# Kernel optimization log

Measured on AMD Instinct MI355X. Metric: run time of the kernel, lower is better.

The kernel has to match this reference:

```python
import jax, jax.numpy as jnp
import numpy as np

DIM = 1024


def setup_inputs() -> dict:
    key = jax.random.key(0)
    ks = jax.random.split(key, 9)
    s = 1.0 / np.sqrt(DIM)
    x = jax.random.normal(ks[0], (4, 4096, DIM), dtype=jnp.float32)
    Wq = jax.random.uniform(ks[1], (DIM, DIM), jnp.float32, -s, s)
    bq = jax.random.uniform(ks[2], (DIM,), jnp.float32, -s, s)
    Wk = jax.random.uniform(ks[3], (DIM, DIM), jnp.float32, -s, s)
    bk = jax.random.uniform(ks[4], (DIM,), jnp.float32, -s, s)
    Wv = jax.random.uniform(ks[5], (DIM, DIM), jnp.float32, -s, s)
    bv = jax.random.uniform(ks[6], (DIM,), jnp.float32, -s, s)
    Wo = jax.random.uniform(ks[7], (DIM, DIM), jnp.float32, -s, s)
    bo = jax.random.uniform(ks[8], (DIM,), jnp.float32, -s, s)
    return {"x": x, "Wq": Wq, "bq": bq, "Wk": Wk, "bk": bk,
            "Wv": Wv, "bv": bv, "Wo": Wo, "bo": bo}


def reference(x, Wq, bq, Wk, bk, Wv, bv, Wo, bo):
    # x: [B, N, C]; weights stored as [C, C] (torch Linear applies x @ W.T,
    # here we store W already transposed so x @ W matches).
    scale = x.shape[-1] ** (-0.5)
    q = x @ Wq + bq                                  # [B, N, C]
    k = x @ Wk + bk
    v = x @ Wv + bv
    scores = jnp.einsum('bnc,bmc->bnm', q, k) * scale  # [B, N, N]
    attn = jax.nn.softmax(scores, axis=-1)
    out = jnp.einsum('bnm,bmc->bnc', attn, v)          # [B, N, C]
    return out @ Wo + bo
```

## Files before the change

### kernel.cpp

```cpp
#include <hip/hip_runtime.h>
#include <hip/hip_bf16.h>
#include <stdint.h>

typedef __bf16 bf16_8 __attribute__((ext_vector_type(8)));
typedef float  f32x4  __attribute__((ext_vector_type(4)));

#define GLL(g, l) __builtin_amdgcn_global_load_lds(                         \
    (__attribute__((address_space(1))) void*)(g),                           \
    (__attribute__((address_space(3))) void*)(l), 16, 0, 0)

__global__ void sniff_dtype(const uint32_t* __restrict__ x, uint32_t* __restrict__ flag)
{
    uint32_t w = x[threadIdx.x];
    uint32_t e = (w >> 23) & 0xFF;
    int isf32 = (e >= 100 && e <= 145) ? 1 : 0;
    unsigned long long m = __ballot(isf32);
    if (threadIdx.x == 0) *flag = (__popcll(m) >= 48) ? 1u : 0u;
}

__global__ __launch_bounds__(256)
void convert_to_bf16(const void* __restrict__ in, long elemOff,
                     __bf16* __restrict__ out, long n, const uint32_t* __restrict__ flag)
{
    long i = ((long)blockIdx.x * 256 + threadIdx.x) * 8;
    if (i >= n) return;
    bf16_8 o;
    if (*flag) {
        const float* p = (const float*)in + elemOff + i;
        float4 a = *(const float4*)p;
        float4 b = *(const float4*)(p + 4);
        o[0]=(__bf16)a.x; o[1]=(__bf16)a.y; o[2]=(__bf16)a.z; o[3]=(__bf16)a.w;
        o[4]=(__bf16)b.x; o[5]=(__bf16)b.y; o[6]=(__bf16)b.z; o[7]=(__bf16)b.w;
    } else {
        o = *(const bf16_8*)((const __bf16*)in + elemOff + i);
    }
    *(bf16_8*)(out + i) = o;
}

__global__ __launch_bounds__(256)
void convert_bias4(const void* b0, const void* b1, const void* b2, const void* b3,
                   __bf16* o0, __bf16* o1, __bf16* o2, __bf16* o3,
                   const uint32_t* __restrict__ flag)
{
    const void* in = (blockIdx.x == 0) ? b0 : (blockIdx.x == 1) ? b1
                   : (blockIdx.x == 2) ? b2 : b3;
    __bf16* out = (blockIdx.x == 0) ? o0 : (blockIdx.x == 1) ? o1
                : (blockIdx.x == 2) ? o2 : o3;
    long i = (long)threadIdx.x * 8;
    if (i >= 1024) return;
    bf16_8 o;
    if (*flag) {
        const float* p = (const float*)in + i;
        float4 a = *(const float4*)p;
        float4 b = *(const float4*)(p + 4);
        o[0]=(__bf16)a.x; o[1]=(__bf16)a.y; o[2]=(__bf16)a.z; o[3]=(__bf16)a.w;
        o[4]=(__bf16)b.x; o[5]=(__bf16)b.y; o[6]=(__bf16)b.z; o[7]=(__bf16)b.w;
    } else {
        o = *(const bf16_8*)((const __bf16*)in + i);
    }
    *(bf16_8*)(out + i) = o;
}

__global__ __launch_bounds__(256)
void convT_w4(const void* W0, const void* W1, const void* W2, const void* W3,
              __bf16* T0, __bf16* T1, __bf16* T2, __bf16* T3,
              const uint32_t* __restrict__ flag)
{
    const void* W = (blockIdx.z == 0) ? W0 : (blockIdx.z == 1) ? W1
                  : (blockIdx.z == 2) ? W2 : W3;
    __bf16* WT    = (blockIdx.z == 0) ? T0 : (blockIdx.z == 1) ? T1
                  : (blockIdx.z == 2) ? T2 : T3;
    __shared__ __bf16 tile[64][72];
    const int bc = blockIdx.x * 64, br = blockIdx.y * 64;
    const int c = threadIdx.x & 63, r0 = threadIdx.x >> 6;
    const bool f32 = (*flag != 0);
#pragma unroll
    for (int i = 0; i < 16; i++) {
        int r = i * 4 + r0;
        long idx = (long)(br + r) * 1024 + bc + c;
        float v = f32 ? ((const float*)W)[idx] : (float)((const __bf16*)W)[idx];
        tile[r][c] = (__bf16)v;
    }
    __syncthreads();
#pragma unroll
    for (int i = 0; i < 16; i++) {
        int r = i * 4 + r0;
        WT[(long)(bc + r) * 1024 + br + c] = tile[c][r];
    }
}

template<int BN_T, int OUT_MODE, bool HAS_BIAS>
__global__ __launch_bounds__(256)
void gemm_bt(const __bf16* __restrict__ A, int lda,
             const __bf16* __restrict__ BT, int ldb,
             void* __restrict__ C, int ldc,
             const __bf16* __restrict__ bias,
             int M, int N, int kLen, long zCbytes, float scale,
             float* __restrict__ rowSums)
{
    constexpr int NT    = (BN_T == 128) ? 4 : 2;
    constexpr int BHALF = BN_T * 32;
    __shared__ __align__(16) __bf16 As[2 * 128 * 32];
    __shared__ __align__(16) __bf16 Bs[2 * BHALF];

    const int t    = threadIdx.x;
    const int wave = t >> 6;
    const int lane = t & 63;
    const int quad = lane >> 4;
    const int lrow = lane & 15;
    const int wm   = wave >> 1;
    const int wn   = wave & 1;
    const long m0  = (long)blockIdx.y * 128;
    const long n0  = (long)blockIdx.x * BN_T;

    A  += (long)blockIdx.z * kLen;
    BT += (long)blockIdx.z * kLen;
    C   = (void*)((char*)C + (long)blockIdx.z * zCbytes);

    const int sr = lane >> 2;
    const int sc = (lane & 3) ^ ((lane >> 3) & 3);

    const __bf16* aSrc = A + (m0 + wave * 32 + sr) * (long)lda + sc * 8;
    const __bf16* bSrc = (BN_T == 128)
        ? BT + (n0 + wave * 32 + sr) * (long)ldb + sc * 8
        : BT + (n0 + wave * 16 + sr) * (long)ldb + sc * 8;
    __bf16* aDst = As + wave * 1024;
    __bf16* bDst = Bs + wave * (BN_T == 128 ? 1024 : 512);
    const long a16 = 16L * lda, b16 = 16L * ldb;

    f32x4 zero4 = {0.f, 0.f, 0.f, 0.f};
    f32x4 acc[4][NT];
#pragma unroll
    for (int mt = 0; mt < 4; mt++)
#pragma unroll
        for (int nt = 0; nt < NT; nt++) acc[mt][nt] = zero4;

    const int sl = (lrow >> 1) & 3;

    for (int k0 = 0; k0 < kLen; k0 += 64) {
        GLL(aSrc, aDst);
        GLL(aSrc + a16, aDst + 512);
        GLL(bSrc, bDst);
        if (BN_T == 128) GLL(bSrc + b16, bDst + 512);
        GLL(aSrc + 32, aDst + 4096);
        GLL(aSrc + a16 + 32, aDst + 4096 + 512);
        GLL(bSrc + 32, bDst + BHALF);
        if (BN_T == 128) GLL(bSrc + b16 + 32, bDst + BHALF + 512);
        aSrc += 64; bSrc += 64;
        __syncthreads();

#pragma unroll
        for (int kk = 0; kk < 2; kk++) {
            bf16_8 af[4], bfr[NT];
#pragma unroll
            for (int mt = 0; mt < 4; mt++)
                af[mt] = *(const bf16_8*)(As + kk * 4096
                           + (wm * 64 + mt * 16 + lrow) * 32 + (quad ^ sl) * 8);
#pragma unroll
            for (int nt = 0; nt < NT; nt++)
                bfr[nt] = *(const bf16_8*)(Bs + kk * BHALF
                           + (wn * (BN_T / 2) + nt * 16 + lrow) * 32 + (quad ^ sl) * 8);

#pragma unroll
            for (int mt = 0; mt < 4; mt++)
#pragma unroll
                for (int nt = 0; nt < NT; nt++)
                    acc[mt][nt] = __builtin_amdgcn_mfma_f32_16x16x32_bf16(
                                      af[mt], bfr[nt], acc[mt][nt], 0, 0, 0);
        }
        __syncthreads();
    }

    if (OUT_MODE == 3) {
#pragma unroll
        for (int mt = 0; mt < 4; mt++) {
#pragma unroll
            for (int i = 0; i < 4; i++) {
                long row = m0 + wm * 64 + mt * 16 + quad * 4 + i;
                float rs = 0.f;
#pragma unroll
                for (int nt = 0; nt < NT; nt++) {
                    long col = n0 + wn * (BN_T / 2) + nt * 16 + lrow;
                    float e = exp2f(acc[mt][nt][i] * scale);
                    ((__bf16*)C)[row * (long)ldc + col] = (__bf16)e;
                    rs += e;
                }
                rs += __shfl_xor(rs, 1);
                rs += __shfl_xor(rs, 2);
                rs += __shfl_xor(rs, 4);
                rs += __shfl_xor(rs, 8);
                if (lrow == 0) atomicAdd(&rowSums[row], rs);
            }
        }
        return;
    }

#pragma unroll
    for (int mt = 0; mt < 4; mt++) {
#pragma unroll
        for (int nt = 0; nt < NT; nt++) {
#pragma unroll
            for (int i = 0; i < 4; i++) {
                long row = m0 + wm * 64 + mt * 16 + quad * 4 + i;
                long col = n0 + wn * (BN_T / 2) + nt * 16 + lrow;
                float v = acc[mt][nt][i] * scale;
                if (HAS_BIAS) v += (float)bias[col];
                if (OUT_MODE == 0)      ((__bf16*)C)[row * (long)ldc + col] = (__bf16)v;
                else if (OUT_MODE == 1) ((__bf16*)C)[col * (long)ldc + row] = (__bf16)v;
                else                    ((float* )C)[row * (long)ldc + col] = v;
            }
        }
    }
}

__global__ __launch_bounds__(256)
void softmax_f32_to_bf16(float* __restrict__ S)
{
    float* srow = S + (long)blockIdx.x * 4096;
    __bf16* prow = (__bf16*)srow;
    const int t  = threadIdx.x;
    const int wv = t >> 6, ln = t & 63;

    float4 vv[4];
    float m = -1e30f;
#pragma unroll
    for (int i = 0; i < 4; i++) {
        vv[i] = ((const float4*)srow)[t + i * 256];
        m = fmaxf(m, fmaxf(fmaxf(vv[i].x, vv[i].y), fmaxf(vv[i].z, vv[i].w)));
    }
#pragma unroll
    for (int o = 32; o; o >>= 1) m = fmaxf(m, __shfl_xor(m, o));
    __shared__ float redm[4];
    if (ln == 0) redm[wv] = m;
    __syncthreads();
    m = fmaxf(fmaxf(redm[0], redm[1]), fmaxf(redm[2], redm[3]));

    const float L2E = 1.4426950408889634f;
    float s = 0.f;
#pragma unroll
    for (int i = 0; i < 4; i++) {
        vv[i].x = exp2f((vv[i].x - m) * L2E);
        vv[i].y = exp2f((vv[i].y - m) * L2E);
        vv[i].z = exp2f((vv[i].z - m) * L2E);
        vv[i].w = exp2f((vv[i].w - m) * L2E);
        s += vv[i].x + vv[i].y + vv[i].z + vv[i].w;
    }
#pragma unroll
    for (int o = 32; o; o >>= 1) s += __shfl_xor(s, o);
    __shared__ float reds[4];
    if (ln == 0) reds[wv] = s;
    __syncthreads();
    s = reds[0] + reds[1] + reds[2] + reds[3];
    float inv = 1.f / s;

    __syncthreads();
#pragma unroll
    for (int i = 0; i < 4; i++) {
        long base = (long)(t + i * 256) * 4;
        prow[base + 0] = (__bf16)(vv[i].x * inv);
        prow[base + 1] = (__bf16)(vv[i].y * inv);
        prow[base + 2] = (__bf16)(vv[i].z * inv);
        prow[base + 3] = (__bf16)(vv[i].w * inv);
    }
}

__global__ __launch_bounds__(256)
void reduce2_to_bf16(const float* __restrict__ Sf, __bf16* __restrict__ ao)
{
    const long i = blockIdx.x;
    const float* p = Sf + 4096 * i + 2048;
    const int t = threadIdx.x;
    float4 a = ((const float4*)p)[t];
    float4 b = ((const float4*)(p + 1024))[t];
    __bf16* o = ao + i * 1024 + t * 4;
    o[0] = (__bf16)(a.x + b.x);
    o[1] = (__bf16)(a.y + b.y);
    o[2] = (__bf16)(a.z + b.z);
    o[3] = (__bf16)(a.w + b.w);
}

__global__ __launch_bounds__(256)
void reduce2_scaled(const float* __restrict__ part, const float* __restrict__ sums,
                    __bf16* __restrict__ ao)
{
    const long i = blockIdx.x;
    const float inv = 1.0f / sums[i];
    const float* p = part + i * 2048;
    const int t = threadIdx.x;
    float4 a = ((const float4*)p)[t];
    float4 b = ((const float4*)(p + 1024))[t];
    __bf16* o = ao + i * 1024 + t * 4;
    o[0] = (__bf16)((a.x + b.x) * inv);
    o[1] = (__bf16)((a.y + b.y) * inv);
    o[2] = (__bf16)((a.z + b.z) * inv);
    o[3] = (__bf16)((a.w + b.w) * inv);
}

__global__ void fill_const_f32(float* p, long n, float val)
{
    long i = (long)blockIdx.x * 256 + threadIdx.x;
    if (i < n) p[i] = val;
}

extern "C" void kernel_launch(void* const* d_in, const int* in_sizes, int n_in,
                              void* d_out, int out_size, void* d_ws, size_t ws_size,
                              hipStream_t stream)
{
    const void* x  = d_in[0];
    const void* Wq = d_in[1];
    const void* bq = d_in[2];
    const void* Wk = d_in[3];
    const void* bk = d_in[4];
    const void* Wv = d_in[5];
    const void* bv = d_in[6];
    const void* Wo = d_in[7];
    const void* bo = d_in[8];

    const int  Bb = 4, Nn = 4096, Cc = 1024;
    const long seqB = (long)Nn * Cc;
    const long allR = (long)Bb * Nn;

    auto pad = [](size_t b) { return (b + 255) & ~(size_t)255; };
    const size_t szW    = (size_t)Cc * Cc * 2;
    const size_t szBias = (size_t)Cc * 2;
    const size_t szSeq  = (size_t)seqB * 2;
    const size_t szAll  = (size_t)allR * Cc * 2;

    const size_t fixed = pad(256) + 4 * pad(szW) + 4 * pad(szBias) + pad(szAll);
    const size_t needB = fixed + 4 * pad(szSeq);
    const size_t needA = fixed + 4 * pad(szAll);

    dim3 blk(256);

    if (ws_size < needB) {
        float val = 3000.0f + (float)(ws_size >> 20);
        fill_const_f32<<<dim3((out_size + 255) / 256), blk, 0, stream>>>(
            (float*)d_out, out_size, val);
        return;
    }

    const bool batched = (ws_size >= needA);

    char* ws = (char*)d_ws;
    size_t off = 0;
    auto alloc = [&](size_t bytes) -> char* { char* p = ws + off; off += pad(bytes); return p; };

    uint32_t* flag = (uint32_t*)alloc(256);
    __bf16* WqT = (__bf16*)alloc(szW);
    __bf16* WkT = (__bf16*)alloc(szW);
    __bf16* WvT = (__bf16*)alloc(szW);
    __bf16* WoT = (__bf16*)alloc(szW);
    __bf16* bqc = (__bf16*)alloc(szBias);
    __bf16* bkc = (__bf16*)alloc(szBias);
    __bf16* bvc = (__bf16*)alloc(szBias);
    __bf16* boc = (__bf16*)alloc(szBias);
    __bf16* ao  = (__bf16*)alloc(szAll);
    const size_t tierSz = batched ? szAll : szSeq;
    __bf16* xc  = (__bf16*)alloc(tierSz);
    __bf16* q   = (__bf16*)alloc(tierSz);
    __bf16* k   = (__bf16*)alloc(tierSz);
    __bf16* vT  = (__bf16*)alloc(tierSz);

    sniff_dtype<<<dim3(1), dim3(64), 0, stream>>>((const uint32_t*)x, flag);
    convT_w4<<<dim3(16, 16, 4), blk, 0, stream>>>(Wq, Wk, Wv, Wo, WqT, WkT, WvT, WoT, flag);
    convert_bias4<<<dim3(4), blk, 0, stream>>>(bq, bk, bv, bo, bqc, bkc, bvc, boc, flag);

    const float scale    = 0.03125f;
    const float scaleL2E = 0.03125f * 1.4426950408889634f;

    if (batched) {
        convert_to_bf16<<<dim3(allR * Cc / 2048), blk, 0, stream>>>(x, 0, xc, allR * Cc, flag);
        dim3 gProj(Cc / 128, allR / 128);
        gemm_bt<128, 0, true><<<gProj, blk, 0, stream>>>(xc, Cc, WqT, Cc, q,  Cc,  bqc, (int)allR, Cc, Cc, 0, 1.f, nullptr);
        gemm_bt<128, 0, true><<<gProj, blk, 0, stream>>>(xc, Cc, WkT, Cc, k,  Cc,  bkc, (int)allR, Cc, Cc, 0, 1.f, nullptr);
        gemm_bt<128, 1, true><<<gProj, blk, 0, stream>>>(xc, Cc, WvT, Cc, vT, (int)allR, bvc, (int)allR, Cc, Cc, 0, 1.f, nullptr);

        float* sums4 = (float*)xc;
        fill_const_f32<<<dim3(64), blk, 0, stream>>>(sums4, 4L * Nn, 0.f);

        __bf16* P   = (__bf16*)d_out;
        float* part = (float*)((char*)d_out + (size_t)Nn * Nn * 2);

        for (int b = 0; b < Bb; b++) {
            const __bf16* qb  = q + (long)b * seqB;
            const __bf16* kb  = k + (long)b * seqB;
            const __bf16* vTb = vT + (long)b * Nn;
            float* sums = sums4 + (long)b * Nn;

            gemm_bt<128, 3, false><<<dim3(Nn / 128, Nn / 128), blk, 0, stream>>>(
                qb, Cc, kb, Cc, P, Nn, nullptr, Nn, Nn, Cc, 0, scaleL2E, sums);

            gemm_bt<128, 2, false><<<dim3(Cc / 128, Nn / 128, 2), blk, 0, stream>>>(
                P, Nn, vTb, (int)allR, part, 2048,
                nullptr, Nn, Cc, Nn / 2, 4096 , 1.f, nullptr);

            reduce2_scaled<<<dim3(Nn), blk, 0, stream>>>(
                part, sums, ao + (long)b * seqB);
        }
    } else {
        float* S = (float*)d_out;
        for (int b = 0; b < Bb; b++) {
            convert_to_bf16<<<dim3(seqB / 2048), blk, 0, stream>>>(x, b * seqB, xc, seqB, flag);
            dim3 gProj(Cc / 64, Nn / 128);
            gemm_bt<64, 0, true><<<gProj, blk, 0, stream>>>(xc, Cc, WqT, Cc, q,  Cc, bqc, Nn, Cc, Cc, 0, 1.f, nullptr);
            gemm_bt<64, 0, true><<<gProj, blk, 0, stream>>>(xc, Cc, WkT, Cc, k,  Cc, bkc, Nn, Cc, Cc, 0, 1.f, nullptr);
            gemm_bt<64, 1, true><<<gProj, blk, 0, stream>>>(xc, Cc, WvT, Cc, vT, Nn, bvc, Nn, Cc, Cc, 0, 1.f, nullptr);

            gemm_bt<128, 2, false><<<dim3(Nn / 128, Nn / 128), blk, 0, stream>>>(
                q, Cc, k, Cc, S, Nn, nullptr, Nn, Nn, Cc, 0, scale, nullptr);

            softmax_f32_to_bf16<<<dim3(Nn), blk, 0, stream>>>(S);

            gemm_bt<128, 2, false><<<dim3(Cc / 128, Nn / 128, 2), blk, 0, stream>>>(
                (const __bf16*)S, 2 * Nn, vT, Nn, (float*)S + 2048, Nn,
                nullptr, Nn, Cc, Nn / 2, 4096, 1.f, nullptr);

            reduce2_to_bf16<<<dim3(Nn), blk, 0, stream>>>(S, ao + (long)b * seqB);
        }
    }

    gemm_bt<128, 2, true><<<dim3(Cc / 128, (int)(allR / 128)), blk, 0, stream>>>(
        ao, Cc, WoT, Cc, (float*)d_out, Cc, boc, (int)allR, Cc, Cc, 0, 1.f, nullptr);
}
```

Baseline: 847.3 us.

## Double-buffer LDS tiles in bf16 GEMM to overlap global loads with MFMA

Adds a second LDS buffer for the A and B tiles so the direct global-to-LDS loads for the next K step are issued before the MFMA work on the current step. This removes one barrier per iteration and hides load latency behind compute. Wave priority is also raised around the MFMA section. In exchange LDS use per block doubles, which can lower occupancy, and completion of the prefetch relies on the barrier's implicit wait.

```diff
diff --git a/kernel.cpp b/kernel.cpp
--- a/kernel.cpp
+++ b/kernel.cpp
@@ -100,8 +100,8 @@
 {
     constexpr int NT    = (BN_T == 128) ? 4 : 2;
     constexpr int BHALF = BN_T * 32;
-    __shared__ __align__(16) __bf16 As[2 * 128 * 32];
-    __shared__ __align__(16) __bf16 Bs[2 * BHALF];
+    __shared__ __align__(16) __bf16 As[2][2 * 128 * 32];
+    __shared__ __align__(16) __bf16 Bs[2][2 * BHALF];
 
     const int t    = threadIdx.x;
     const int wave = t >> 6;
@@ -124,8 +124,6 @@
     const __bf16* bSrc = (BN_T == 128)
         ? BT + (n0 + wave * 32 + sr) * (long)ldb + sc * 8
         : BT + (n0 + wave * 16 + sr) * (long)ldb + sc * 8;
-    __bf16* aDst = As + wave * 1024;
-    __bf16* bDst = Bs + wave * (BN_T == 128 ? 1024 : 512);
     const long a16 = 16L * lda, b16 = 16L * ldb;
 
     f32x4 zero4 = {0.f, 0.f, 0.f, 0.f};
@@ -137,28 +135,30 @@
 
     const int sl = (lrow >> 1) & 3;
 
-    for (int k0 = 0; k0 < kLen; k0 += 64) {
-        GLL(aSrc, aDst);
-        GLL(aSrc + a16, aDst + 512);
-        GLL(bSrc, bDst);
-        if (BN_T == 128) GLL(bSrc + b16, bDst + 512);
-        GLL(aSrc + 32, aDst + 4096);
-        GLL(aSrc + a16 + 32, aDst + 4096 + 512);
-        GLL(bSrc + 32, bDst + BHALF);
-        if (BN_T == 128) GLL(bSrc + b16 + 32, bDst + BHALF + 512);
-        aSrc += 64; bSrc += 64;
-        __syncthreads();
-
+    auto STAGE = [&](int buf, const __bf16* aS, const __bf16* bS) {
+        __bf16* aD = &As[buf][0] + wave * 1024;
+        __bf16* bD = &Bs[buf][0] + wave * (BN_T == 128 ? 1024 : 512);
+        GLL(aS, aD);
+        GLL(aS + a16, aD + 512);
+        GLL(bS, bD);
+        if (BN_T == 128) GLL(bS + b16, bD + 512);
+        GLL(aS + 32, aD + 4096);
+        GLL(aS + a16 + 32, aD + 4096 + 512);
+        GLL(bS + 32, bD + BHALF);
+        if (BN_T == 128) GLL(bS + b16 + 32, bD + BHALF + 512);
+    };
+
+    auto COMPUTE = [&](int buf) {
 #pragma unroll
         for (int kk = 0; kk < 2; kk++) {
             bf16_8 af[4], bfr[NT];
 #pragma unroll
             for (int mt = 0; mt < 4; mt++)
-                af[mt] = *(const bf16_8*)(As + kk * 4096
+                af[mt] = *(const bf16_8*)(&As[buf][0] + kk * 4096
                            + (wm * 64 + mt * 16 + lrow) * 32 + (quad ^ sl) * 8);
 #pragma unroll
             for (int nt = 0; nt < NT; nt++)
-                bfr[nt] = *(const bf16_8*)(Bs + kk * BHALF
+                bfr[nt] = *(const bf16_8*)(&Bs[buf][0] + kk * BHALF
                            + (wn * (BN_T / 2) + nt * 16 + lrow) * 32 + (quad ^ sl) * 8);
 
 #pragma unroll
@@ -168,8 +168,25 @@
                     acc[mt][nt] = __builtin_amdgcn_mfma_f32_16x16x32_bf16(
                                       af[mt], bfr[nt], acc[mt][nt], 0, 0, 0);
         }
+    };
+
+    STAGE(0, aSrc, bSrc);
+    aSrc += 64; bSrc += 64;
+    __syncthreads();
+
+    int cur = 0;
+    for (int k0 = 64; k0 < kLen; k0 += 64) {
+        STAGE(cur ^ 1, aSrc, bSrc);
+        aSrc += 64; bSrc += 64;
+        __builtin_amdgcn_s_setprio(1);
+        COMPUTE(cur);
+        __builtin_amdgcn_s_setprio(0);
         __syncthreads();
-    }
+        cur ^= 1;
+    }
+    __builtin_amdgcn_s_setprio(1);
+    COMPUTE(cur);
+    __builtin_amdgcn_s_setprio(0);
 
     if (OUT_MODE == 3) {
 #pragma unroll
```

New measurement: 776.1 us. 8.4% less time.
